# Optimization experiments

Measured on AMD Instinct MI355X. Metric: run time of the kernel, lower is better.

## Reference

```python
import jax, jax.numpy as jnp
import numpy as np

P_SIZES = (1, 2, 4)
O_SIZE = 32
EPS = 1e-5


def bilin_matrix(S, O):
    """Interpolation matrix (O, S) for torch UpsamplingBilinear2d (align_corners=True)."""
    if S == 1:
        return jnp.ones((O, 1), dtype=jnp.float32)
    pos = jnp.arange(O, dtype=jnp.float32) * ((S - 1) / (O - 1))
    lo = jnp.clip(jnp.floor(pos).astype(jnp.int32), 0, S - 2)
    frac = pos - lo.astype(jnp.float32)
    rows = jnp.arange(O)
    M = jnp.zeros((O, S), dtype=jnp.float32)
    M = M.at[rows, lo].add(1.0 - frac).at[rows, lo + 1].add(frac)
    return M


def setup_inputs() -> dict:
    key = jax.random.key(0)
    ks = jax.random.split(key, 12)
    n, C, H = 16, 512, 32
    c4 = C // 4      # 128, value/pyramid channels
    qk = c4 // 8     # 16, query/key channels inside SAE
    s = 0.05
    return {
        "x": jax.random.normal(ks[0], (n, C, H, H), jnp.float32),
        "rce_w": jax.random.normal(ks[1], (3, c4, C), jnp.float32) * s,   # 1x1 conv per pyramid scale
        "rce_b": jax.random.normal(ks[2], (3, c4), jnp.float32) * s,
        "q_w": jax.random.normal(ks[3], (qk, c4), jnp.float32) * s,       # SAE query 1x1 conv
        "q_b": jax.random.normal(ks[4], (qk,), jnp.float32) * s,
        "k_w": jax.random.normal(ks[5], (qk, c4), jnp.float32) * s,       # SAE key 1x1 conv
        "k_b": jax.random.normal(ks[6], (qk,), jnp.float32) * s,
        "value_w": jax.random.normal(ks[7], (c4, C), jnp.float32) * s,    # value 1x1 conv
        "value_b": jax.random.normal(ks[8], (c4,), jnp.float32) * s,
        "fusion_w": jax.random.normal(ks[9], (C, 3 * c4, 3, 3), jnp.float32) * s,  # 3x3 conv, no bias
        "bn_scale": 1.0 + jax.random.normal(ks[10], (C,), jnp.float32) * s,
        "bn_bias": jax.random.normal(ks[11], (C,), jnp.float32) * s,
        "gamma": jnp.asarray(0.5, jnp.float32),
    }


def reference(x, rce_w, rce_b, q_w, q_b, k_w, k_b, value_w, value_b,
              fusion_w, bn_scale, bn_bias, gamma):
    n, C, H, W = x.shape
    c4 = C // 4
    L = H * W

    # value projection: 1x1 conv then flatten -> (n, c4, L)
    proj_value = (jnp.einsum('oc,nchw->nohw', value_w, x)
                  + value_b[None, :, None, None]).reshape(n, c4, L)

    outs = []
    for i, sz in enumerate(P_SIZES):
        # AdaptiveAvgPool2d((sz, sz)) with divisible input -> exact uniform pooling
        pooled = x.reshape(n, C, sz, H // sz, sz, W // sz).mean(axis=(3, 5))
        # 1x1 conv C -> c4
        feat = jnp.einsum('oc,ncij->noij', rce_w[i], pooled) + rce_b[i][None, :, None, None]
        # bilinear upsample (align_corners=True) to (O_SIZE, O_SIZE)
        M = bilin_matrix(sz, O_SIZE)
        up = jnp.einsum('oi,pj,ncij->ncop', M, M, feat)  # (n, c4, H, W)
        # SAE: query/key 1x1 convs, flatten, bmm + softmax
        q = (jnp.einsum('oc,nchw->nohw', q_w, up) + q_b[None, :, None, None]).reshape(n, -1, L)
        k = (jnp.einsum('oc,nchw->nohw', k_w, up) + k_b[None, :, None, None]).reshape(n, -1, L)
        energy = jnp.einsum('ncl,ncm->nlm', q, k)        # (n, L, L)
        attn = jax.nn.softmax(energy, axis=-1)
        # temp = bmm(value, attn^T): temp[c,m] = sum_l value[c,l] * attn[m,l]
        outs.append(jnp.einsum('ncl,nml->ncm', proj_value, attn).reshape(n, c4, H, W))

    cat = jnp.concatenate(outs, axis=1)                  # (n, 3*c4, H, W)
    y = jax.lax.conv_general_dilated(
        cat, fusion_w, window_strides=(1, 1), padding=((1, 1), (1, 1)),
        dimension_numbers=('NCHW', 'OIHW', 'NCHW'))
    # BatchNorm2d in training mode (default): batch statistics over (N, H, W)
    mean = y.mean(axis=(0, 2, 3))
    var = y.var(axis=(0, 2, 3))
    y = (y - mean[None, :, None, None]) * (bn_scale / jnp.sqrt(var + EPS))[None, :, None, None] \
        + bn_bias[None, :, None, None]
    y = jax.nn.relu(y)
    return gamma * y + x
```

## Files before the change

### kernel.cpp

```cpp
#include <hip/hip_runtime.h>
#include <hip/hip_fp16.h>
#include <math.h>

#define OFF_COR   0u
#define OFF_PVH   2097152u
#define OFF_Y     3145728u
#define OFF_CATP  11534336u
#define OFF_QH    15085568u
#define OFF_KH    15347712u
#define OFF_POOL  16134144u
#define OFF_FEAT  16297984u
#define OFF_AW    16338944u
#define OFF_MEANS 17223680u
#define OFF_STAT  17225728u
#define OFF_VWH   17226752u

typedef __bf16 bf16x8 __attribute__((ext_vector_type(8)));
typedef _Float16 f16x8 __attribute__((ext_vector_type(8)));
typedef _Float16 f16x4 __attribute__((ext_vector_type(4)));
typedef float f32x4 __attribute__((ext_vector_type(4)));

__device__ __forceinline__ unsigned short f2bf(float f) {
  unsigned int u = __float_as_uint(f);
  unsigned int r = u + 0x7fff + ((u >> 16) & 1);
  return (unsigned short)(r >> 16);
}

__device__ __forceinline__ unsigned short f2h(float f) {
  union { _Float16 h; unsigned short u; } cv;
  cv.h = (_Float16)f;
  return cv.u;
}

__device__ __forceinline__ void gload_lds16(const void* g, void* l) {
  __builtin_amdgcn_global_load_lds(
      (const __attribute__((address_space(1))) unsigned int*)g,
      (__attribute__((address_space(3))) unsigned int*)l, 16, 0, 0);
}

__global__ __launch_bounds__(256) void pool_kernel(const float* __restrict__ x,
                                                   float* __restrict__ pool) {
  int b = blockIdx.x;
  int t = threadIdx.x;
  const float4* xp = (const float4*)(x + (size_t)b * 1024);
  float4 v = xp[t];
  float s4 = v.x + v.y + v.z + v.w;
  __shared__ float sm[256];
  __shared__ float p4s[16];
  sm[t] = s4;
  __syncthreads();
  if (t < 16) {
    int br = t >> 2, bc = t & 3;
    float s = 0.f;
#pragma unroll
    for (int rr = 0; rr < 8; ++rr) {
      int base = br * 64 + rr * 8 + bc * 2;
      s += sm[base] + sm[base + 1];
    }
    s *= (1.f / 64.f);
    p4s[t] = s;
    pool[(size_t)b * 20 + t] = s;
  }
  __syncthreads();
  if (t < 4) {
    int i2 = t >> 1, j2 = t & 1;
    float s = (p4s[(2*i2)*4 + 2*j2]     + p4s[(2*i2)*4 + 2*j2 + 1] +
               p4s[(2*i2+1)*4 + 2*j2]   + p4s[(2*i2+1)*4 + 2*j2 + 1]) * 0.25f;
    pool[(size_t)b * 20 + 16 + t] = s;
  }
}

__global__ __launch_bounds__(64) void feat_kernel(const float* __restrict__ pool,
                                                  const float* __restrict__ rce_w,
                                                  const float* __restrict__ rce_b,
                                                  float* __restrict__ feat) {
  int o = blockIdx.x, n = blockIdx.y, t = threadIdx.x;
  float part[20];
#pragma unroll
  for (int j = 0; j < 20; ++j) part[j] = 0.f;
  for (int c = t; c < 512; c += 64) {
    const float* pl = pool + ((size_t)n * 512 + c) * 20;
    float w2 = rce_w[(size_t)(128 + o) * 512 + c];
    float w4 = rce_w[(size_t)(256 + o) * 512 + c];
#pragma unroll
    for (int j = 0; j < 4; ++j)  part[j]     += w2 * pl[16 + j];
#pragma unroll
    for (int j = 0; j < 16; ++j) part[4 + j] += w4 * pl[j];
  }
  __shared__ float red[64][20];
#pragma unroll
  for (int j = 0; j < 20; ++j) red[t][j] = part[j];
  __syncthreads();
  if (t < 20) {
    float s = 0.f;
    for (int i = 0; i < 64; ++i) s += red[i][t];
    s += (t < 4) ? rce_b[128 + o] : rce_b[256 + o];
    feat[((size_t)n * 128 + o) * 20 + t] = s;
  }
}

__global__ __launch_bounds__(256) void qk2_kernel(const float* __restrict__ feat,
                                                  const float* __restrict__ q_w,
                                                  const float* __restrict__ q_b,
                                                  const float* __restrict__ k_w,
                                                  const float* __restrict__ k_b,
                                                  unsigned short* __restrict__ qh,
                                                  unsigned short* __restrict__ kh) {
  int n = blockIdx.x, t = threadIdx.x;
  __shared__ float fL[128 * 20];
  __shared__ float GH[2][16][20];
  for (int idx = t; idx < 2560; idx += 256) fL[idx] = feat[(size_t)n * 2560 + idx];
  __syncthreads();
  for (int idx = t; idx < 640; idx += 256) {
    int which = idx / 320, rem = idx % 320, qc = rem / 20, j = rem % 20;
    const float* w = which ? k_w : q_w;
    float s = which ? k_b[qc] : q_b[qc];
    for (int c = 0; c < 128; ++c) s += w[qc * 128 + c] * fL[c * 20 + j];
    GH[which][qc][j] = s;
  }
  __syncthreads();
  for (int it = 0; it < 16; ++it) {
    int row = t + 256 * it;
    int l = row & 1023, which = (row >> 10) & 1, s = row >> 11;
    int ry = l >> 5, cx = l & 31;
    int t0, t1, t2, t3;
    float w0, w1, w2, w3;
    if (s == 0) {
      float a = ry * (1.0f / 31.0f), b = cx * (1.0f / 31.0f);
      t0 = 0; t1 = 1; t2 = 2; t3 = 3;
      w0 = (1.f - a) * (1.f - b); w1 = (1.f - a) * b;
      w2 = a * (1.f - b);         w3 = a * b;
    } else {
      float pr = ry * (3.0f / 31.0f);
      int lr = (int)pr; if (lr > 2) lr = 2;
      float fr = pr - (float)lr;
      float pc = cx * (3.0f / 31.0f);
      int lc = (int)pc; if (lc > 2) lc = 2;
      float fc = pc - (float)lc;
      int base = 4 + lr * 4 + lc;
      t0 = base; t1 = base + 1; t2 = base + 4; t3 = base + 5;
      w0 = (1.f - fr) * (1.f - fc); w1 = (1.f - fr) * fc;
      w2 = fr * (1.f - fc);         w3 = fr * fc;
    }
    float val[16];
#pragma unroll
    for (int qc = 0; qc < 16; ++qc) {
      const float* G = GH[which][qc];
      val[qc] = w0 * G[t0] + w1 * G[t1] + w2 * G[t2] + w3 * G[t3];
    }
    unsigned short* dst = (which ? kh : qh) + (((size_t)(s * 16 + n) * 1024 + l) * 16);
#pragma unroll
    for (int u = 0; u < 4; ++u)
      *(ushort4*)(dst + 4 * u) = make_ushort4(f2h(val[4*u]), f2h(val[4*u+1]),
                                              f2h(val[4*u+2]), f2h(val[4*u+3]));
  }
}

__global__ __launch_bounds__(256) void xcast_kernel(const float* __restrict__ x,
                                                    unsigned short* __restrict__ xT) {
  int lt = blockIdx.x, ct = blockIdx.y, n = blockIdx.z;
  int l0 = lt * 64, c0 = ct * 64, t = threadIdx.x;
  __shared__ float tile[64 * 65];
#pragma unroll
  for (int i = 0; i < 16; ++i) {
    int idx = t + 256 * i;
    int c = idx >> 6, l = idx & 63;
    tile[c * 65 + l] = x[((size_t)n * 512 + c0 + c) * 1024 + l0 + l];
  }
  __syncthreads();
#pragma unroll
  for (int i = 0; i < 16; ++i) {
    int idx = t + 256 * i;
    int l = idx >> 6, c = idx & 63;
    xT[((size_t)n * 1024 + l0 + l) * 512 + c0 + c] = f2h(tile[c * 65 + l]);
  }
}

__global__ __launch_bounds__(256) void vwcast_kernel(const float* __restrict__ vw,
                                                     unsigned short* __restrict__ vwh) {
  int i = blockIdx.x * 256 + threadIdx.x;
  vwh[i] = f2h(vw[i]);
}

__global__ __launch_bounds__(256) void pvmm2_kernel(const unsigned short* __restrict__ vwh,
                                                    const unsigned short* __restrict__ xT,
                                                    const float* __restrict__ vb,
                                                    unsigned short* __restrict__ pvh) {
  int l0 = blockIdx.x * 64;
  int n = blockIdx.y;
  int t = threadIdx.x, lane = t & 63, wv = t >> 6;
  int wm = (wv & 1) * 64, wn = (wv >> 1) * 32;

  __shared__ short Asm[128 * 32];
  __shared__ short Bsm[64 * 32];

  int ar0 = t >> 2,        aq0 = (t & 3) ^ ((ar0 >> 1) & 3);
  int idx1 = t + 256; int ar1 = idx1 >> 2, aq1 = (idx1 & 3) ^ ((ar1 >> 1) & 3);
  int br  = t >> 2,        bq  = (t & 3) ^ ((br >> 1) & 3);
  const unsigned short* Ab0 = vwh + (size_t)ar0 * 512 + aq0 * 8;
  const unsigned short* Ab1 = vwh + (size_t)ar1 * 512 + aq1 * 8;
  const unsigned short* Bb  = xT + ((size_t)n * 1024 + l0 + br) * 512 + bq * 8;
  char* ldsA = (char*)Asm;
  char* ldsB = (char*)Bsm;
  int wvoff = wv * 1024;
  int r15 = lane & 15, kg = lane >> 4;
  int kq = kg ^ ((r15 >> 1) & 3);

  f32x4 acc[4][2];
#pragma unroll
  for (int i = 0; i < 4; ++i)
#pragma unroll
    for (int j = 0; j < 2; ++j) acc[i][j] = (f32x4){0.f, 0.f, 0.f, 0.f};

  for (int k0 = 0; k0 < 512; k0 += 32) {
    __syncthreads();
    gload_lds16(Ab0 + k0, ldsA + wvoff);
    gload_lds16(Ab1 + k0, ldsA + 4096 + wvoff);
    gload_lds16(Bb + k0,  ldsB + wvoff);
    __syncthreads();
    f16x8 af[4], bfr[2];
#pragma unroll
    for (int mt2 = 0; mt2 < 4; ++mt2)
      af[mt2] = *(const f16x8*)&Asm[(wm + mt2 * 16 + r15) * 32 + kq * 8];
#pragma unroll
    for (int nt2 = 0; nt2 < 2; ++nt2)
      bfr[nt2] = *(const f16x8*)&Bsm[(wn + nt2 * 16 + r15) * 32 + kq * 8];
#pragma unroll
    for (int mt2 = 0; mt2 < 4; ++mt2)
#pragma unroll
      for (int nt2 = 0; nt2 < 2; ++nt2)
        acc[mt2][nt2] = __builtin_amdgcn_mfma_f32_16x16x32_f16(af[mt2], bfr[nt2], acc[mt2][nt2], 0, 0, 0);
  }

  int c_lo = wm + (lane >> 4) * 4;
  int l_lo = wn + (lane & 15);
#pragma unroll
  for (int mt2 = 0; mt2 < 4; ++mt2)
#pragma unroll
    for (int nt2 = 0; nt2 < 2; ++nt2) {
      int l = l0 + l_lo + nt2 * 16;
#pragma unroll
      for (int r = 0; r < 4; ++r) {
        int c = c_lo + mt2 * 16 + r;
        pvh[((size_t)n * 128 + c) * 1024 + l] = f2h(acc[mt2][nt2][r] + vb[c]);
      }
    }
}

__global__ __launch_bounds__(256) void mean_kernel(const unsigned short* __restrict__ pvh,
                                                   float* __restrict__ means) {
  int c = blockIdx.x, n = blockIdx.y, t = threadIdx.x;
  f16x4 v = ((const f16x4*)(pvh + ((size_t)n * 128 + c) * 1024))[t];
  float s = (float)v[0] + (float)v[1] + (float)v[2] + (float)v[3];
  for (int o = 32; o > 0; o >>= 1) s += __shfl_down(s, o);
  __shared__ float wsum[4];
  if ((t & 63) == 0) wsum[t >> 6] = s;
  __syncthreads();
  if (t == 0) means[n * 128 + c] = (wsum[0] + wsum[1] + wsum[2] + wsum[3]) * (1.f / 1024.f);
}

__global__ __launch_bounds__(64) void basecor_kernel(const float* __restrict__ means,
                                                     const float* __restrict__ fw,
                                                     float* __restrict__ cor) {
  int oc = blockIdx.x, n = blockIdx.y, t = threadIdx.x;
  float S[9];
#pragma unroll
  for (int j = 0; j < 9; ++j) S[j] = 0.f;
  for (int c = t; c < 128; c += 64) {
    float m = means[n * 128 + c];
    const float* wp = fw + (size_t)oc * 3456 + c * 9;
#pragma unroll
    for (int j = 0; j < 9; ++j) S[j] += m * wp[j];
  }
  __shared__ float red[64][9];
  __shared__ float Sf[9];
#pragma unroll
  for (int j = 0; j < 9; ++j) red[t][j] = S[j];
  __syncthreads();
  if (t < 9) {
    float s = 0.f;
    for (int i = 0; i < 64; ++i) s += red[i][t];
    Sf[t] = s;
  }
  __syncthreads();
  if (t < 9) {
    int a = t / 3, b = t % 3;
    float s = 0.f;
#pragma unroll
    for (int ky = 0; ky < 3; ++ky) {
      if ((a == 0 && ky == 0) || (a == 2 && ky == 2)) continue;
#pragma unroll
      for (int kx = 0; kx < 3; ++kx) {
        if ((b == 0 && kx == 0) || (b == 2 && kx == 2)) continue;
        s += Sf[ky * 3 + kx];
      }
    }
    cor[((size_t)n * 512 + oc) * 9 + t] = s;
  }
}

__global__ __launch_bounds__(128) void fillcat_kernel(unsigned short* __restrict__ catp) {
  int b = blockIdx.x;
  int n = b / 132, e = b % 132;
  int py, px;
  if (e < 34)       { py = 0;          px = e; }
  else if (e < 68)  { py = 33;         px = e - 34; }
  else if (e < 100) { py = e - 68 + 1; px = 0; }
  else              { py = e - 100 + 1; px = 33; }
  unsigned int* row = (unsigned int*)(catp + ((size_t)n * 1156 + py * 34 + px) * 256);
  row[threadIdx.x] = 0u;
}

__global__ __launch_bounds__(256) void wcast_kernel(const float* __restrict__ fw,
                                                    unsigned short* __restrict__ Aw) {
  int oc = blockIdx.x, t = threadIdx.x;
  for (int j = t; j < 2304; j += 256) {
    int seg = j >> 8, ic2 = j & 255;
    Aw[(size_t)oc * 2304 + j] = f2bf(fw[(size_t)oc * 3456 + (128 + ic2) * 9 + seg]);
  }
}

__global__ __launch_bounds__(256) void fattn_kernel(const unsigned short* __restrict__ qh,
                                                    const unsigned short* __restrict__ kh,
                                                    const unsigned short* __restrict__ pvh,
                                                    unsigned short* __restrict__ catp) {
  int m0 = blockIdx.x * 64;
  int n = blockIdx.y, sc = blockIdx.z;
  int t = threadIdx.x, lane = t & 63, wv = t >> 6;
  int wc = (wv >> 1) * 64;
  int wm2 = (wv & 1) * 32;
  int r15 = lane & 15, kg = lane >> 4;
  int kq = kg ^ ((r15 >> 1) & 3);

  const unsigned short* qb  = qh + ((size_t)(sc * 16 + n) * 1024 + m0 + wv * 16) * 16;
  const unsigned short* kb  = kh + ((size_t)(sc * 16 + n) * 1024) * 16;
  const unsigned short* pvb = pvh + (size_t)n * 128 * 1024;

  __shared__ short PVs[2 * 128 * 32];
  __shared__ _Float16 Us[64 * 72];
  __shared__ float rsum[64];

  f16x8 zf = {0, 0, 0, 0, 0, 0, 0, 0};
  f16x8 qa = (kg < 2) ? *(const f16x8*)(qb + r15 * 16 + kg * 8) : zf;

  int prow = t >> 2;
  int aq = (t & 3) ^ ((prow >> 1) & 3);
  const unsigned short* Pb0 = pvb + (size_t)prow * 1024 + aq * 8;
  const unsigned short* Pb1 = pvb + (size_t)(prow + 64) * 1024 + aq * 8;
  char* ldsPV = (char*)PVs;
  int wvoff = wv * 1024;

  f32x4 acc[4][2];
#pragma unroll
  for (int i = 0; i < 4; ++i)
#pragma unroll
    for (int j = 0; j < 2; ++j) acc[i][j] = (f32x4){0.f, 0.f, 0.f, 0.f};
  float rs[4] = {0.f, 0.f, 0.f, 0.f};

  for (int it = 0; it < 16; ++it) {
    int l0 = it * 64;
    __syncthreads();
    gload_lds16(Pb0 + l0,      ldsPV + wvoff);
    gload_lds16(Pb1 + l0,      ldsPV + 4096 + wvoff);
    gload_lds16(Pb0 + l0 + 32, ldsPV + 8192 + wvoff);
    gload_lds16(Pb1 + l0 + 32, ldsPV + 12288 + wvoff);

    f32x4 sacc[4];
#pragma unroll
    for (int lt = 0; lt < 4; ++lt) {
      f16x8 kbf = (kg < 2)
        ? *(const f16x8*)(kb + (size_t)(l0 + lt * 16 + r15) * 16 + kg * 8) : zf;
      sacc[lt] = __builtin_amdgcn_mfma_f32_16x16x32_f16(qa, kbf, (f32x4){0.f,0.f,0.f,0.f}, 0, 0, 0);
    }
#pragma unroll
    for (int lt = 0; lt < 4; ++lt)
#pragma unroll
      for (int r = 0; r < 4; ++r) {
        float e = __expf(sacc[lt][r]);
        Us[(wv * 16 + kg * 4 + r) * 72 + lt * 16 + r15] = (_Float16)e;
        rs[r] += e;
      }
    __syncthreads();

#pragma unroll
    for (int ks = 0; ks < 2; ++ks) {
      f16x8 bfr[2];
#pragma unroll
      for (int nt = 0; nt < 2; ++nt)
        bfr[nt] = *(const f16x8*)&Us[(wm2 + nt * 16 + r15) * 72 + ks * 32 + kg * 8];
#pragma unroll
      for (int ct = 0; ct < 4; ++ct) {
        f16x8 af = *(const f16x8*)&PVs[ks * 4096 + (wc + ct * 16 + r15) * 32 + kq * 8];
#pragma unroll
        for (int nt = 0; nt < 2; ++nt)
          acc[ct][nt] = __builtin_amdgcn_mfma_f32_16x16x32_f16(af, bfr[nt], acc[ct][nt], 0, 0, 0);
      }
    }
  }

#pragma unroll
  for (int r = 0; r < 4; ++r) {
    rs[r] += __shfl_xor(rs[r], 1);
    rs[r] += __shfl_xor(rs[r], 2);
    rs[r] += __shfl_xor(rs[r], 4);
    rs[r] += __shfl_xor(rs[r], 8);
  }
  if (r15 == 0) {
#pragma unroll
    for (int r = 0; r < 4; ++r) rsum[wv * 16 + kg * 4 + r] = rs[r];
  }
  __syncthreads();

#pragma unroll
  for (int nt = 0; nt < 2; ++nt) {
    float inv = 1.f / rsum[wm2 + nt * 16 + r15];
    int pix = m0 + wm2 + nt * 16 + r15;
    unsigned short* ob = catp + ((size_t)n * 1156 + ((pix >> 5) + 1) * 34 + (pix & 31) + 1) * 256
                       + sc * 128 + wc + kg * 4;
#pragma unroll
    for (int ct = 0; ct < 4; ++ct) {
      ushort4 o = make_ushort4(f2bf(acc[ct][nt][0] * inv), f2bf(acc[ct][nt][1] * inv),
                               f2bf(acc[ct][nt][2] * inv), f2bf(acc[ct][nt][3] * inv));
      *(ushort4*)(ob + ct * 16) = o;
    }
  }
}

__global__ __launch_bounds__(256) void convmm_kernel(const unsigned short* __restrict__ Aw,
                                                     const unsigned short* __restrict__ catp,
                                                     const float* __restrict__ cor,
                                                     float* __restrict__ y) {
  int ntile = blockIdx.x;
  int n = ntile >> 3, y0 = (ntile & 7) * 4;
  int m0 = blockIdx.y * 128;
  int t = threadIdx.x;
  int lane = t & 63, wv = t >> 6;
  int wm = (wv & 1) * 64, wn = (wv >> 1) * 64;

  __shared__ short Asm[128 * 32];
  __shared__ short Bsm[128 * 32];

  int idx0 = t, idx1 = t + 256;
  int ar0 = idx0 >> 2, aq0 = (idx0 & 3) ^ ((ar0 >> 1) & 3);
  int ar1 = idx1 >> 2, aq1 = (idx1 & 3) ^ ((ar1 >> 1) & 3);
  size_t abase0 = (size_t)(m0 + ar0) * 2304 + aq0 * 8;
  size_t abase1 = (size_t)(m0 + ar1) * 2304 + aq1 * 8;
  size_t bbase0 = ((size_t)n * 1156 + (size_t)(y0 + (ar0 >> 5)) * 34 + (ar0 & 31)) * 256 + aq0 * 8;
  size_t bbase1 = ((size_t)n * 1156 + (size_t)(y0 + (ar1 >> 5)) * 34 + (ar1 & 31)) * 256 + aq1 * 8;
  char* ldsA = (char*)Asm;
  char* ldsB = (char*)Bsm;
  int wvoff = wv * 1024;

  int r15 = lane & 15, kg = lane >> 4;
  int kq = kg ^ ((r15 >> 1) & 3);

  f32x4 acc[4][4];
#pragma unroll
  for (int i = 0; i < 4; ++i)
#pragma unroll
    for (int j = 0; j < 4; ++j) acc[i][j] = (f32x4){0.f, 0.f, 0.f, 0.f};

  for (int seg = 0; seg < 9; ++seg) {
    size_t boffseg = (size_t)((seg / 3) * 34 + (seg % 3)) * 256;
    size_t akkseg = (size_t)seg * 256;
    for (int icc = 0; icc < 8; ++icc) {
      size_t akk = akkseg + icc * 32;
      size_t boff = boffseg + icc * 32;
      __syncthreads();
      gload_lds16(Aw + abase0 + akk,   ldsA + wvoff);
      gload_lds16(Aw + abase1 + akk,   ldsA + 4096 + wvoff);
      gload_lds16(catp + bbase0 + boff, ldsB + wvoff);
      gload_lds16(catp + bbase1 + boff, ldsB + 4096 + wvoff);
      __syncthreads();
      bf16x8 af[4], bf[4];
#pragma unroll
      for (int mt = 0; mt < 4; ++mt)
        af[mt] = *(const bf16x8*)&Asm[(wm + mt * 16 + r15) * 32 + kq * 8];
#pragma unroll
      for (int nt = 0; nt < 4; ++nt)
        bf[nt] = *(const bf16x8*)&Bsm[(wn + nt * 16 + r15) * 32 + kq * 8];
#pragma unroll
      for (int mt = 0; mt < 4; ++mt)
#pragma unroll
        for (int nt = 0; nt < 4; ++nt)
          acc[mt][nt] = __builtin_amdgcn_mfma_f32_16x16x32_bf16(af[mt], bf[nt], acc[mt][nt], 0, 0, 0);
    }
  }

  int pixbase = (ntile & 7) * 128 + wn + (lane & 15);
  int ocbase = m0 + wm + (lane >> 4) * 4;
#pragma unroll
  for (int mt = 0; mt < 4; ++mt)
#pragma unroll
    for (int nt = 0; nt < 4; ++nt) {
      int oc = ocbase + mt * 16;
      int pix = pixbase + nt * 16;
      int py = pix >> 5, px = pix & 31;
      int yc = (py == 0) ? 0 : ((py == 31) ? 2 : 1);
      int xc = (px == 0) ? 0 : ((px == 31) ? 2 : 1);
      const float* cp = cor + ((size_t)n * 512 + oc) * 9 + yc * 3 + xc;
      float* yp = y + ((size_t)n * 512 + oc) * 1024 + pix;
#pragma unroll
      for (int r = 0; r < 4; ++r) yp[(size_t)r * 1024] = acc[mt][nt][r] + cp[(size_t)r * 9];
    }
}

__global__ __launch_bounds__(256) void bnstat_kernel(const float* __restrict__ y,
                                                     const float* __restrict__ bn_scale,
                                                     const float* __restrict__ bn_bias,
                                                     float* __restrict__ stats) {
  int oc = blockIdx.x, t = threadIdx.x;
  float s = 0.f, ss = 0.f;
  for (int n = 0; n < 16; ++n) {
    float4 v = ((const float4*)(y + ((size_t)n * 512 + oc) * 1024))[t];
    s  += v.x + v.y + v.z + v.w;
    ss += v.x * v.x + v.y * v.y + v.z * v.z + v.w * v.w;
  }
  for (int o = 32; o > 0; o >>= 1) {
    s  += __shfl_down(s, o);
    ss += __shfl_down(ss, o);
  }
  __shared__ float rs[4], rss[4];
  if ((t & 63) == 0) { rs[t >> 6] = s; rss[t >> 6] = ss; }
  __syncthreads();
  if (t == 0) {
    float S = rs[0] + rs[1] + rs[2] + rs[3];
    float SS = rss[0] + rss[1] + rss[2] + rss[3];
    float mean = S * (1.f / 16384.f);
    float var = SS * (1.f / 16384.f) - mean * mean;
    float se = bn_scale[oc] / sqrtf(var + 1e-5f);
    stats[oc * 2] = se;
    stats[oc * 2 + 1] = bn_bias[oc] - mean * se;
  }
}

__global__ __launch_bounds__(256) void final_kernel(const float* __restrict__ y,
                                                    const float* __restrict__ x,
                                                    const float* __restrict__ stats,
                                                    const float* __restrict__ gamma,
                                                    float* __restrict__ outp) {
  int b = blockIdx.x;
  int c = b & 511;
  int t = threadIdx.x;
  float se = stats[c * 2], sh = stats[c * 2 + 1], g = gamma[0];
  float4 yv = ((const float4*)(y + (size_t)b * 1024))[t];
  float4 xv = ((const float4*)(x + (size_t)b * 1024))[t];
  float4 o;
  o.x = g * fmaxf(yv.x * se + sh, 0.f) + xv.x;
  o.y = g * fmaxf(yv.y * se + sh, 0.f) + xv.y;
  o.z = g * fmaxf(yv.z * se + sh, 0.f) + xv.z;
  o.w = g * fmaxf(yv.w * se + sh, 0.f) + xv.w;
  ((float4*)(outp + (size_t)b * 1024))[t] = o;
}

extern "C" void kernel_launch(void* const* d_in, const int* in_sizes, int n_in,
                              void* d_out, int out_size, void* d_ws, size_t ws_size,
                              hipStream_t stream) {
  const float* x        = (const float*)d_in[0];
  const float* rce_w    = (const float*)d_in[1];
  const float* rce_b    = (const float*)d_in[2];
  const float* q_w      = (const float*)d_in[3];
  const float* q_b      = (const float*)d_in[4];
  const float* k_w      = (const float*)d_in[5];
  const float* k_b      = (const float*)d_in[6];
  const float* value_w  = (const float*)d_in[7];
  const float* value_b  = (const float*)d_in[8];
  const float* fw       = (const float*)d_in[9];
  const float* bn_scale = (const float*)d_in[10];
  const float* bn_bias  = (const float*)d_in[11];
  const float* gamma    = (const float*)d_in[12];

  float* ws    = (float*)d_ws;
  float* cor   = ws + OFF_COR;
  unsigned short* pvh = (unsigned short*)(ws + OFF_PVH);
  float* ybuf  = ws + OFF_Y;
  unsigned short* xTbuf = (unsigned short*)(ws + OFF_Y);
  unsigned short* catp = (unsigned short*)(ws + OFF_CATP);
  unsigned short* qh   = (unsigned short*)(ws + OFF_QH);
  unsigned short* kh   = (unsigned short*)(ws + OFF_KH);
  float* pool  = ws + OFF_POOL;
  float* feat  = ws + OFF_FEAT;
  unsigned short* Aw = (unsigned short*)(ws + OFF_AW);
  float* means = ws + OFF_MEANS;
  float* stats = ws + OFF_STAT;
  unsigned short* vwh = (unsigned short*)(ws + OFF_VWH);
  float* outp  = (float*)d_out;

  hipLaunchKernelGGL(pool_kernel,    dim3(8192),       dim3(256), 0, stream, x, pool);
  hipLaunchKernelGGL(feat_kernel,    dim3(128, 16),    dim3(64),  0, stream, pool, rce_w, rce_b, feat);
  hipLaunchKernelGGL(qk2_kernel,     dim3(16),         dim3(256), 0, stream, feat, q_w, q_b, k_w, k_b, qh, kh);
  hipLaunchKernelGGL(xcast_kernel,   dim3(16, 8, 16),  dim3(256), 0, stream, x, xTbuf);
  hipLaunchKernelGGL(vwcast_kernel,  dim3(256),        dim3(256), 0, stream, value_w, vwh);
  hipLaunchKernelGGL(pvmm2_kernel,   dim3(16, 16),     dim3(256), 0, stream, vwh, xTbuf, value_b, pvh);
  hipLaunchKernelGGL(mean_kernel,    dim3(128, 16),    dim3(256), 0, stream, pvh, means);
  hipLaunchKernelGGL(basecor_kernel, dim3(512, 16),    dim3(64),  0, stream, means, fw, cor);
  hipLaunchKernelGGL(fillcat_kernel, dim3(2112),       dim3(128), 0, stream, catp);
  hipLaunchKernelGGL(wcast_kernel,   dim3(512),        dim3(256), 0, stream, fw, Aw);
  hipLaunchKernelGGL(fattn_kernel,   dim3(16, 16, 2),  dim3(256), 0, stream, qh, kh, pvh, catp);
  hipLaunchKernelGGL(convmm_kernel,  dim3(128, 4),     dim3(256), 0, stream, Aw, catp, cor, ybuf);
  hipLaunchKernelGGL(bnstat_kernel,  dim3(512),        dim3(256), 0, stream, ybuf, bn_scale, bn_bias, stats);
  hipLaunchKernelGGL(final_kernel,   dim3(8192),       dim3(256), 0, stream, ybuf, x, stats, gamma, outp);
}
```

Baseline: 264.9 us.

## Merge prep kernels, fuse mean and BN statistics into GEMM epilogues, store y in fp16

Several small preparation kernels (pooling, x transpose-cast, weight casts, border zero-fill, stat clearing) are merged into one launch that branches on block index. The per-channel mean of the value projection and the BN sum and sum of squares are now accumulated with atomics in the pvmm and convmm epilogues, which removes the separate mean and bnstat passes. The conv output is stored in fp16 instead of fp32, so the final pass reads less data. The qk2 kernel is spread over more blocks. The cost is extra atomic contention and lower precision in the intermediate y and in the variance computed as E[y²]-mean².

```diff
diff --git a/kernel.cpp b/kernel.cpp
--- a/kernel.cpp
+++ b/kernel.cpp
@@ -38,35 +38,87 @@
       (__attribute__((address_space(3))) unsigned int*)l, 16, 0, 0);
 }
 
-__global__ __launch_bounds__(256) void pool_kernel(const float* __restrict__ x,
-                                                   float* __restrict__ pool) {
+__global__ __launch_bounds__(256) void prep_kernel(const float* __restrict__ x,
+                                                   const float* __restrict__ vw,
+                                                   const float* __restrict__ fw,
+                                                   float* __restrict__ pool,
+                                                   unsigned short* __restrict__ xT,
+                                                   unsigned short* __restrict__ vwh,
+                                                   unsigned short* __restrict__ Aw,
+                                                   unsigned short* __restrict__ catp,
+                                                   float* __restrict__ stats,
+                                                   float* __restrict__ means) {
   int b = blockIdx.x;
   int t = threadIdx.x;
-  const float4* xp = (const float4*)(x + (size_t)b * 1024);
-  float4 v = xp[t];
-  float s4 = v.x + v.y + v.z + v.w;
-  __shared__ float sm[256];
-  __shared__ float p4s[16];
-  sm[t] = s4;
-  __syncthreads();
-  if (t < 16) {
-    int br = t >> 2, bc = t & 3;
-    float s = 0.f;
-#pragma unroll
-    for (int rr = 0; rr < 8; ++rr) {
-      int base = br * 64 + rr * 8 + bc * 2;
-      s += sm[base] + sm[base + 1];
-    }
-    s *= (1.f / 64.f);
-    p4s[t] = s;
-    pool[(size_t)b * 20 + t] = s;
-  }
-  __syncthreads();
-  if (t < 4) {
-    int i2 = t >> 1, j2 = t & 1;
-    float s = (p4s[(2*i2)*4 + 2*j2]     + p4s[(2*i2)*4 + 2*j2 + 1] +
-               p4s[(2*i2+1)*4 + 2*j2]   + p4s[(2*i2+1)*4 + 2*j2 + 1]) * 0.25f;
-    pool[(size_t)b * 20 + 16 + t] = s;
+  __shared__ float smem[64 * 65];
+  if (b < 8192) {
+    const float4* xp = (const float4*)(x + (size_t)b * 1024);
+    float4 v = xp[t];
+    float s4 = v.x + v.y + v.z + v.w;
+    float* sm = smem;
+    float* p4s = smem + 256;
+    sm[t] = s4;
+    __syncthreads();
+    if (t < 16) {
+      int br = t >> 2, bc = t & 3;
+      float s = 0.f;
+#pragma unroll
+      for (int rr = 0; rr < 8; ++rr) {
+        int base = br * 64 + rr * 8 + bc * 2;
+        s += sm[base] + sm[base + 1];
+      }
+      s *= (1.f / 64.f);
+      p4s[t] = s;
+      pool[(size_t)b * 20 + t] = s;
+    }
+    __syncthreads();
+    if (t < 4) {
+      int i2 = t >> 1, j2 = t & 1;
+      float s = (p4s[(2*i2)*4 + 2*j2]     + p4s[(2*i2)*4 + 2*j2 + 1] +
+                 p4s[(2*i2+1)*4 + 2*j2]   + p4s[(2*i2+1)*4 + 2*j2 + 1]) * 0.25f;
+      pool[(size_t)b * 20 + 16 + t] = s;
+    }
+  } else if (b < 10240) {
+    int u = b - 8192;
+    int lt = u & 15, ct = (u >> 4) & 7, n = u >> 7;
+    int l0 = lt * 64, c0 = ct * 64;
+#pragma unroll
+    for (int i = 0; i < 16; ++i) {
+      int idx = t + 256 * i;
+      int c = idx >> 6, l = idx & 63;
+      smem[c * 65 + l] = x[((size_t)n * 512 + c0 + c) * 1024 + l0 + l];
+    }
+    __syncthreads();
+#pragma unroll
+    for (int i = 0; i < 16; ++i) {
+      int idx = t + 256 * i;
+      int l = idx >> 6, c = idx & 63;
+      xT[((size_t)n * 1024 + l0 + l) * 512 + c0 + c] = f2h(smem[c * 65 + l]);
+    }
+  } else if (b < 10496) {
+    int i = (b - 10240) * 256 + t;
+    vwh[i] = f2h(vw[i]);
+  } else if (b < 11008) {
+    int oc = b - 10496;
+    for (int j = t; j < 2304; j += 256) {
+      int seg = j >> 8, ic2 = j & 255;
+      Aw[(size_t)oc * 2304 + j] = f2bf(fw[(size_t)oc * 3456 + (128 + ic2) * 9 + seg]);
+    }
+  } else if (b < 12064) {
+    int rr = (b - 11008) * 2 + (t >> 7);
+    int n = rr / 132, e = rr % 132;
+    int py, px;
+    if (e < 34)       { py = 0;           px = e; }
+    else if (e < 68)  { py = 33;          px = e - 34; }
+    else if (e < 100) { py = e - 68 + 1;  px = 0; }
+    else              { py = e - 100 + 1; px = 33; }
+    unsigned int* row = (unsigned int*)(catp + ((size_t)n * 1156 + py * 34 + px) * 256);
+    row[t & 127] = 0u;
+  } else {
+    for (int i = t; i < 3072; i += 256) {
+      if (i < 1024) stats[i] = 0.f;
+      else means[i - 1024] = 0.f;
+    }
   }
 }
 
@@ -106,7 +158,7 @@
                                                   const float* __restrict__ k_b,
                                                   unsigned short* __restrict__ qh,
                                                   unsigned short* __restrict__ kh) {
-  int n = blockIdx.x, t = threadIdx.x;
+  int n = blockIdx.x, chunk = blockIdx.y, t = threadIdx.x;
   __shared__ float fL[128 * 20];
   __shared__ float GH[2][16][20];
   for (int idx = t; idx < 2560; idx += 256) fL[idx] = feat[(size_t)n * 2560 + idx];
@@ -119,17 +171,17 @@
     GH[which][qc][j] = s;
   }
   __syncthreads();
-  for (int it = 0; it < 16; ++it) {
-    int row = t + 256 * it;
+  {
+    int row = t + 256 * chunk;
     int l = row & 1023, which = (row >> 10) & 1, s = row >> 11;
     int ry = l >> 5, cx = l & 31;
     int t0, t1, t2, t3;
     float w0, w1, w2, w3;
     if (s == 0) {
-      float a = ry * (1.0f / 31.0f), b = cx * (1.0f / 31.0f);
+      float a = ry * (1.0f / 31.0f), b2 = cx * (1.0f / 31.0f);
       t0 = 0; t1 = 1; t2 = 2; t3 = 3;
-      w0 = (1.f - a) * (1.f - b); w1 = (1.f - a) * b;
-      w2 = a * (1.f - b);         w3 = a * b;
+      w0 = (1.f - a) * (1.f - b2); w1 = (1.f - a) * b2;
+      w2 = a * (1.f - b2);         w3 = a * b2;
     } else {
       float pr = ry * (3.0f / 31.0f);
       int lr = (int)pr; if (lr > 2) lr = 2;
@@ -156,36 +208,11 @@
   }
 }
 
-__global__ __launch_bounds__(256) void xcast_kernel(const float* __restrict__ x,
-                                                    unsigned short* __restrict__ xT) {
-  int lt = blockIdx.x, ct = blockIdx.y, n = blockIdx.z;
-  int l0 = lt * 64, c0 = ct * 64, t = threadIdx.x;
-  __shared__ float tile[64 * 65];
-#pragma unroll
-  for (int i = 0; i < 16; ++i) {
-    int idx = t + 256 * i;
-    int c = idx >> 6, l = idx & 63;
-    tile[c * 65 + l] = x[((size_t)n * 512 + c0 + c) * 1024 + l0 + l];
-  }
-  __syncthreads();
-#pragma unroll
-  for (int i = 0; i < 16; ++i) {
-    int idx = t + 256 * i;
-    int l = idx >> 6, c = idx & 63;
-    xT[((size_t)n * 1024 + l0 + l) * 512 + c0 + c] = f2h(tile[c * 65 + l]);
-  }
-}
-
-__global__ __launch_bounds__(256) void vwcast_kernel(const float* __restrict__ vw,
-                                                     unsigned short* __restrict__ vwh) {
-  int i = blockIdx.x * 256 + threadIdx.x;
-  vwh[i] = f2h(vw[i]);
-}
-
 __global__ __launch_bounds__(256) void pvmm2_kernel(const unsigned short* __restrict__ vwh,
                                                     const unsigned short* __restrict__ xT,
                                                     const float* __restrict__ vb,
-                                                    unsigned short* __restrict__ pvh) {
+                                                    unsigned short* __restrict__ pvh,
+                                                    float* __restrict__ means) {
   int l0 = blockIdx.x * 64;
   int n = blockIdx.y;
   int t = threadIdx.x, lane = t & 63, wv = t >> 6;
@@ -232,31 +259,24 @@
         acc[mt2][nt2] = __builtin_amdgcn_mfma_f32_16x16x32_f16(af[mt2], bfr[nt2], acc[mt2][nt2], 0, 0, 0);
   }
 
-  int c_lo = wm + (lane >> 4) * 4;
-  int l_lo = wn + (lane & 15);
+  int c_lo = wm + kg * 4;
+  int l_lo = wn + r15;
 #pragma unroll
   for (int mt2 = 0; mt2 < 4; ++mt2)
 #pragma unroll
-    for (int nt2 = 0; nt2 < 2; ++nt2) {
-      int l = l0 + l_lo + nt2 * 16;
-#pragma unroll
-      for (int r = 0; r < 4; ++r) {
-        int c = c_lo + mt2 * 16 + r;
-        pvh[((size_t)n * 128 + c) * 1024 + l] = f2h(acc[mt2][nt2][r] + vb[c]);
-      }
-    }
-}
-
-__global__ __launch_bounds__(256) void mean_kernel(const unsigned short* __restrict__ pvh,
-                                                   float* __restrict__ means) {
-  int c = blockIdx.x, n = blockIdx.y, t = threadIdx.x;
-  f16x4 v = ((const f16x4*)(pvh + ((size_t)n * 128 + c) * 1024))[t];
-  float s = (float)v[0] + (float)v[1] + (float)v[2] + (float)v[3];
-  for (int o = 32; o > 0; o >>= 1) s += __shfl_down(s, o);
-  __shared__ float wsum[4];
-  if ((t & 63) == 0) wsum[t >> 6] = s;
-  __syncthreads();
-  if (t == 0) means[n * 128 + c] = (wsum[0] + wsum[1] + wsum[2] + wsum[3]) * (1.f / 1024.f);
+    for (int r = 0; r < 4; ++r) {
+      int c = c_lo + mt2 * 16 + r;
+      float bias = vb[c];
+      float v0 = acc[mt2][0][r] + bias;
+      float v1 = acc[mt2][1][r] + bias;
+      unsigned short* pp = pvh + ((size_t)n * 128 + c) * 1024 + l0 + l_lo;
+      pp[0]  = f2h(v0);
+      pp[16] = f2h(v1);
+      float s = v0 + v1;
+      s += __shfl_xor(s, 1); s += __shfl_xor(s, 2);
+      s += __shfl_xor(s, 4); s += __shfl_xor(s, 8);
+      if (r15 == 0) atomicAdd(&means[n * 128 + c], s);
+    }
 }
 
 __global__ __launch_bounds__(64) void basecor_kernel(const float* __restrict__ means,
@@ -267,7 +287,7 @@
 #pragma unroll
   for (int j = 0; j < 9; ++j) S[j] = 0.f;
   for (int c = t; c < 128; c += 64) {
-    float m = means[n * 128 + c];
+    float m = means[n * 128 + c] * (1.f / 1024.f);
     const float* wp = fw + (size_t)oc * 3456 + c * 9;
 #pragma unroll
     for (int j = 0; j < 9; ++j) S[j] += m * wp[j];
@@ -296,27 +316,6 @@
       }
     }
     cor[((size_t)n * 512 + oc) * 9 + t] = s;
-  }
-}
-
-__global__ __launch_bounds__(128) void fillcat_kernel(unsigned short* __restrict__ catp) {
-  int b = blockIdx.x;
-  int n = b / 132, e = b % 132;
-  int py, px;
-  if (e < 34)       { py = 0;          px = e; }
-  else if (e < 68)  { py = 33;         px = e - 34; }
-  else if (e < 100) { py = e - 68 + 1; px = 0; }
-  else              { py = e - 100 + 1; px = 33; }
-  unsigned int* row = (unsigned int*)(catp + ((size_t)n * 1156 + py * 34 + px) * 256);
-  row[threadIdx.x] = 0u;
-}
-
-__global__ __launch_bounds__(256) void wcast_kernel(const float* __restrict__ fw,
-                                                    unsigned short* __restrict__ Aw) {
-  int oc = blockIdx.x, t = threadIdx.x;
-  for (int j = t; j < 2304; j += 256) {
-    int seg = j >> 8, ic2 = j & 255;
-    Aw[(size_t)oc * 2304 + j] = f2bf(fw[(size_t)oc * 3456 + (128 + ic2) * 9 + seg]);
   }
 }
 
@@ -429,7 +428,8 @@
 __global__ __launch_bounds__(256) void convmm_kernel(const unsigned short* __restrict__ Aw,
                                                      const unsigned short* __restrict__ catp,
                                                      const float* __restrict__ cor,
-                                                     float* __restrict__ y) {
+                                                     unsigned short* __restrict__ yh,
+                                                     float* __restrict__ stats) {
   int ntile = blockIdx.x;
   int n = ntile >> 3, y0 = (ntile & 7) * 4;
   int m0 = blockIdx.y * 128;
@@ -487,69 +487,61 @@
     }
   }
 
-  int pixbase = (ntile & 7) * 128 + wn + (lane & 15);
-  int ocbase = m0 + wm + (lane >> 4) * 4;
+  int pixbase = (ntile & 7) * 128 + wn + r15;
+  int ocb = m0 + wm + kg * 4;
 #pragma unroll
   for (int mt = 0; mt < 4; ++mt)
 #pragma unroll
-    for (int nt = 0; nt < 4; ++nt) {
-      int oc = ocbase + mt * 16;
-      int pix = pixbase + nt * 16;
-      int py = pix >> 5, px = pix & 31;
-      int yc = (py == 0) ? 0 : ((py == 31) ? 2 : 1);
-      int xc = (px == 0) ? 0 : ((px == 31) ? 2 : 1);
-      const float* cp = cor + ((size_t)n * 512 + oc) * 9 + yc * 3 + xc;
-      float* yp = y + ((size_t)n * 512 + oc) * 1024 + pix;
-#pragma unroll
-      for (int r = 0; r < 4; ++r) yp[(size_t)r * 1024] = acc[mt][nt][r] + cp[(size_t)r * 9];
-    }
-}
-
-__global__ __launch_bounds__(256) void bnstat_kernel(const float* __restrict__ y,
-                                                     const float* __restrict__ bn_scale,
-                                                     const float* __restrict__ bn_bias,
-                                                     float* __restrict__ stats) {
-  int oc = blockIdx.x, t = threadIdx.x;
-  float s = 0.f, ss = 0.f;
-  for (int n = 0; n < 16; ++n) {
-    float4 v = ((const float4*)(y + ((size_t)n * 512 + oc) * 1024))[t];
-    s  += v.x + v.y + v.z + v.w;
-    ss += v.x * v.x + v.y * v.y + v.z * v.z + v.w * v.w;
-  }
-  for (int o = 32; o > 0; o >>= 1) {
-    s  += __shfl_down(s, o);
-    ss += __shfl_down(ss, o);
-  }
-  __shared__ float rs[4], rss[4];
-  if ((t & 63) == 0) { rs[t >> 6] = s; rss[t >> 6] = ss; }
-  __syncthreads();
-  if (t == 0) {
-    float S = rs[0] + rs[1] + rs[2] + rs[3];
-    float SS = rss[0] + rss[1] + rss[2] + rss[3];
-    float mean = S * (1.f / 16384.f);
-    float var = SS * (1.f / 16384.f) - mean * mean;
-    float se = bn_scale[oc] / sqrtf(var + 1e-5f);
-    stats[oc * 2] = se;
-    stats[oc * 2 + 1] = bn_bias[oc] - mean * se;
-  }
-}
-
-__global__ __launch_bounds__(256) void final_kernel(const float* __restrict__ y,
+    for (int r = 0; r < 4; ++r) {
+      int oc = ocb + mt * 16 + r;
+      const float* cp = cor + ((size_t)n * 512 + oc) * 9;
+      unsigned short* yp = yh + ((size_t)n * 512 + oc) * 1024;
+      float s = 0.f, q = 0.f;
+#pragma unroll
+      for (int nt = 0; nt < 4; ++nt) {
+        int pix = pixbase + nt * 16;
+        int py = pix >> 5, px = pix & 31;
+        int yc = (py == 0) ? 0 : ((py == 31) ? 2 : 1);
+        int xc = (px == 0) ? 0 : ((px == 31) ? 2 : 1);
+        float yv = acc[mt][nt][r] + cp[yc * 3 + xc];
+        yp[pix] = f2h(yv);
+        s += yv;
+        q += yv * yv;
+      }
+      s += __shfl_xor(s, 1); s += __shfl_xor(s, 2);
+      s += __shfl_xor(s, 4); s += __shfl_xor(s, 8);
+      q += __shfl_xor(q, 1); q += __shfl_xor(q, 2);
+      q += __shfl_xor(q, 4); q += __shfl_xor(q, 8);
+      if (r15 == 0) {
+        atomicAdd(&stats[oc], s);
+        atomicAdd(&stats[512 + oc], q);
+      }
+    }
+}
+
+__global__ __launch_bounds__(256) void final_kernel(const unsigned short* __restrict__ yh,
                                                     const float* __restrict__ x,
                                                     const float* __restrict__ stats,
+                                                    const float* __restrict__ bn_scale,
+                                                    const float* __restrict__ bn_bias,
                                                     const float* __restrict__ gamma,
                                                     float* __restrict__ outp) {
   int b = blockIdx.x;
   int c = b & 511;
   int t = threadIdx.x;
-  float se = stats[c * 2], sh = stats[c * 2 + 1], g = gamma[0];
-  float4 yv = ((const float4*)(y + (size_t)b * 1024))[t];
+  float sum = stats[c], sq = stats[512 + c];
+  float mean = sum * (1.f / 16384.f);
+  float var = sq * (1.f / 16384.f) - mean * mean;
+  float se = bn_scale[c] / sqrtf(var + 1e-5f);
+  float sh = bn_bias[c] - mean * se;
+  float g = gamma[0];
+  f16x4 yv = ((const f16x4*)(yh + (size_t)b * 1024))[t];
   float4 xv = ((const float4*)(x + (size_t)b * 1024))[t];
   float4 o;
-  o.x = g * fmaxf(yv.x * se + sh, 0.f) + xv.x;
-  o.y = g * fmaxf(yv.y * se + sh, 0.f) + xv.y;
-  o.z = g * fmaxf(yv.z * se + sh, 0.f) + xv.z;
-  o.w = g * fmaxf(yv.w * se + sh, 0.f) + xv.w;
+  o.x = g * fmaxf((float)yv[0] * se + sh, 0.f) + xv.x;
+  o.y = g * fmaxf((float)yv[1] * se + sh, 0.f) + xv.y;
+  o.z = g * fmaxf((float)yv[2] * se + sh, 0.f) + xv.z;
+  o.w = g * fmaxf((float)yv[3] * se + sh, 0.f) + xv.w;
   ((float4*)(outp + (size_t)b * 1024))[t] = o;
 }
 
@@ -573,7 +565,7 @@
   float* ws    = (float*)d_ws;
   float* cor   = ws + OFF_COR;
   unsigned short* pvh = (unsigned short*)(ws + OFF_PVH);
-  float* ybuf  = ws + OFF_Y;
+  unsigned short* yh    = (unsigned short*)(ws + OFF_Y);
   unsigned short* xTbuf = (unsigned short*)(ws + OFF_Y);
   unsigned short* catp = (unsigned short*)(ws + OFF_CATP);
   unsigned short* qh   = (unsigned short*)(ws + OFF_QH);
@@ -586,18 +578,14 @@
   unsigned short* vwh = (unsigned short*)(ws + OFF_VWH);
   float* outp  = (float*)d_out;
 
-  hipLaunchKernelGGL(pool_kernel,    dim3(8192),       dim3(256), 0, stream, x, pool);
+  hipLaunchKernelGGL(prep_kernel,    dim3(12065),      dim3(256), 0, stream,
+                     x, value_w, fw, pool, xTbuf, vwh, Aw, catp, stats, means);
   hipLaunchKernelGGL(feat_kernel,    dim3(128, 16),    dim3(64),  0, stream, pool, rce_w, rce_b, feat);
-  hipLaunchKernelGGL(qk2_kernel,     dim3(16),         dim3(256), 0, stream, feat, q_w, q_b, k_w, k_b, qh, kh);
-  hipLaunchKernelGGL(xcast_kernel,   dim3(16, 8, 16),  dim3(256), 0, stream, x, xTbuf);
-  hipLaunchKernelGGL(vwcast_kernel,  dim3(256),        dim3(256), 0, stream, value_w, vwh);
-  hipLaunchKernelGGL(pvmm2_kernel,   dim3(16, 16),     dim3(256), 0, stream, vwh, xTbuf, value_b, pvh);
-  hipLaunchKernelGGL(mean_kernel,    dim3(128, 16),    dim3(256), 0, stream, pvh, means);
+  hipLaunchKernelGGL(qk2_kernel,     dim3(16, 16),     dim3(256), 0, stream, feat, q_w, q_b, k_w, k_b, qh, kh);
+  hipLaunchKernelGGL(pvmm2_kernel,   dim3(16, 16),     dim3(256), 0, stream, vwh, xTbuf, value_b, pvh, means);
   hipLaunchKernelGGL(basecor_kernel, dim3(512, 16),    dim3(64),  0, stream, means, fw, cor);
-  hipLaunchKernelGGL(fillcat_kernel, dim3(2112),       dim3(128), 0, stream, catp);
-  hipLaunchKernelGGL(wcast_kernel,   dim3(512),        dim3(256), 0, stream, fw, Aw);
   hipLaunchKernelGGL(fattn_kernel,   dim3(16, 16, 2),  dim3(256), 0, stream, qh, kh, pvh, catp);
-  hipLaunchKernelGGL(convmm_kernel,  dim3(128, 4),     dim3(256), 0, stream, Aw, catp, cor, ybuf);
-  hipLaunchKernelGGL(bnstat_kernel,  dim3(512),        dim3(256), 0, stream, ybuf, bn_scale, bn_bias, stats);
-  hipLaunchKernelGGL(final_kernel,   dim3(8192),       dim3(256), 0, stream, ybuf, x, stats, gamma, outp);
-}
+  hipLaunchKernelGGL(convmm_kernel,  dim3(128, 4),     dim3(256), 0, stream, Aw, catp, cor, yh, stats);
+  hipLaunchKernelGGL(final_kernel,   dim3(8192),       dim3(256), 0, stream,
+                     yh, x, stats, bn_scale, bn_bias, gamma, outp);
+}
```

Result: slower. 279.8 us (+5.6%).
